# Performance work log

Measured on AMD Instinct MI355X. Metric: run time of the kernel, lower is better.

## Reference

```python
import jax, jax.numpy as jnp
import numpy as np

TEMPERATURE = 64.0


def setup_inputs() -> dict:
    key = jax.random.key(0)
    k1, k2 = jax.random.split(key)
    B, OUT, C = 256, 1000, 512
    x = jax.random.normal(k1, (B, 1, C), dtype=jnp.float32)
    # weight init: normal(0, sqrt(2/num_classes))
    weight = jax.random.normal(k2, (OUT, C), dtype=jnp.float32) * np.sqrt(2.0 / C).astype(np.float32)
    return {"x": x, "weight": weight, "num_batch": B}


def reference(x, weight, num_batch):
    # weight: (OUT, C) broadcast against x: (B, 1, C)
    # diff intermediate: (B, OUT, C); scores: (B, OUT)
    diff = weight[None, :, :] - x
    scores = -jnp.sum(diff * diff, axis=2) / TEMPERATURE
    return scores
```

## Files before the change

### kernel.cpp

```cpp
#include <hip/hip_runtime.h>
#include <hip/hip_bf16.h>


constexpr int OUTN = 1000;
constexpr int C_   = 512;

typedef __attribute__((ext_vector_type(8))) short bf16x8;
typedef __attribute__((ext_vector_type(4))) float f32x4;

__device__ __forceinline__ unsigned short f2bf(float f) {
    __hip_bfloat16 b = __float2bfloat16(f);
    return *reinterpret_cast<unsigned short*>(&b);
}

__global__ __launch_bounds__(512, 2)
void euc_mfma(const float* __restrict__ x, const float* __restrict__ w,
              float* __restrict__ out) {
    __shared__ unsigned short xs[32][512];
    __shared__ unsigned short ws[32][512];

    const int t    = threadIdx.x;
    const int lane = t & 63;
    const int wv   = t >> 6;
    const int rb   = blockIdx.y * 32;
    const int cb   = blockIdx.x * 32;

    #pragma unroll
    for (int i = 0; i < 8; ++i) {
        const int  row = 8 * (i & 3) + wv;
        const bool isx = (i < 4);
        float4 v0 = make_float4(0.f, 0.f, 0.f, 0.f), v1 = v0;
        if (isx) {
            const float* s = &x[(rb + row) * C_ + lane * 8];
            v0 = *(const float4*)s;  v1 = *(const float4*)(s + 4);
        } else if (cb + row < OUTN) {
            const float* s = &w[(cb + row) * C_ + lane * 8];
            v0 = *(const float4*)s;  v1 = *(const float4*)(s + 4);
        }
        union { unsigned short s[8]; int4 q; } u;
        u.s[0] = f2bf(v0.x); u.s[1] = f2bf(v0.y); u.s[2] = f2bf(v0.z); u.s[3] = f2bf(v0.w);
        u.s[4] = f2bf(v1.x); u.s[5] = f2bf(v1.y); u.s[6] = f2bf(v1.z); u.s[7] = f2bf(v1.w);
        const int g = lane ^ (row & 7);
        if (isx) *(int4*)&xs[row][g * 8] = u.q;
        else     *(int4*)&ws[row][g * 8] = u.q;
    }
    __syncthreads();

    const int q  = wv & 3, h = wv >> 2;
    const int qr = q >> 1, qc = q & 1;
    const int ra = 16 * qr + (lane & 15);
    const int rw = 16 * qc + (lane & 15);

    bf16x8 af[8], bf[8];
    f32x4 acc = {0.f, 0.f, 0.f, 0.f};
    #pragma unroll
    for (int i = 0; i < 8; ++i) {
        const int gi = 32 * h + 4 * i + (lane >> 4);
        af[i] = *(const bf16x8*)&xs[ra][(gi ^ (ra & 7)) * 8];
        bf[i] = *(const bf16x8*)&ws[rw][(gi ^ (rw & 7)) * 8];
        acc = __builtin_amdgcn_mfma_f32_16x16x32_bf16(af[i], bf[i], acc, 0, 0, 0);
    }

    const bool useA = (q == 0) || (q == 3);
    f32x4 nacc = {0.f, 0.f, 0.f, 0.f};
    if (useA) {
        #pragma unroll
        for (int i = 0; i < 8; ++i)
            nacc = __builtin_amdgcn_mfma_f32_16x16x32_bf16(af[i], af[i], nacc, 0, 0, 0);
    } else {
        #pragma unroll
        for (int i = 0; i < 8; ++i)
            nacc = __builtin_amdgcn_mfma_f32_16x16x32_bf16(bf[i], bf[i], nacc, 0, 0, 0);
    }

    __syncthreads();

    char* sbase = (char*)&xs[0][0];
    float* nb = (float*)(sbase + 4096);
    if (h == 1) *(f32x4*)(sbase + q * 1024 + lane * 16) = acc;
    {
        const int base = useA ? 16 * qr : 32 + 16 * qc;
        #pragma unroll
        for (int j = 0; j < 4; ++j) {
            const int r = (lane >> 4) * 4 + j;
            if ((lane & 15) == r) nb[h * 64 + base + r] = nacc[j];
        }
    }
    __syncthreads();

    if (h == 0) {
        const f32x4 p = *(const f32x4*)(sbase + q * 1024 + lane * 16);
        const int cl = 16 * qc + (lane & 15);
        const int c  = cb + cl;
        if (c < OUTN) {
            const float nw = nb[32 + cl] + nb[64 + 32 + cl];
            #pragma unroll
            for (int j = 0; j < 4; ++j) {
                const int r = 16 * qr + (lane >> 4) * 4 + j;
                const float nx = nb[r] + nb[64 + r];
                out[(rb + r) * OUTN + c] =
                    (2.f * (acc[j] + p[j]) - nx - nw) * 0.015625f;
            }
        }
    }
}

extern "C" void kernel_launch(void* const* d_in, const int* in_sizes, int n_in,
                              void* d_out, int out_size, void* d_ws, size_t ws_size,
                              hipStream_t stream) {
    const float* x = (const float*)d_in[0];
    const float* w = (const float*)d_in[1];
    float* out = (float*)d_out;

    dim3 grid((OUTN + 31) / 32, 256 / 32);
    dim3 block(512);
    euc_mfma<<<grid, block, 0, stream>>>(x, w, out);
}
```

Measured before the change: 9.816 us.

## Split K reduction across four wave groups with 1024-thread blocks

Doubles the block to 1024 threads so the 512-wide K dimension is split four ways (16 waves) instead of two, each wave doing half as many MFMAs and LDS reads. The staging loop is rewritten to a flat 4-iteration load over 1024 threads. Partial dot products and norms from the three extra K-slices are reduced through shared memory before the output write. This shortens per-wave serial work at the cost of more cross-wave reduction traffic and higher register and occupancy pressure per block.

```diff
diff --git a/kernel.cpp b/kernel.cpp
--- a/kernel.cpp
+++ b/kernel.cpp
@@ -13,7 +13,7 @@
     return *reinterpret_cast<unsigned short*>(&b);
 }
 
-__global__ __launch_bounds__(512, 2)
+__global__ __launch_bounds__(1024, 4)
 void euc_mfma(const float* __restrict__ x, const float* __restrict__ w,
               float* __restrict__ out) {
     __shared__ unsigned short xs[32][512];
@@ -26,23 +26,24 @@
     const int cb   = blockIdx.x * 32;
 
     #pragma unroll
-    for (int i = 0; i < 8; ++i) {
-        const int  row = 8 * (i & 3) + wv;
-        const bool isx = (i < 4);
+    for (int j = 0; j < 4; ++j) {
+        const int gidx = j * 1024 + t;
+        const int row  = gidx >> 6;
+        const int g    = gidx & 63;
         float4 v0 = make_float4(0.f, 0.f, 0.f, 0.f), v1 = v0;
-        if (isx) {
-            const float* s = &x[(rb + row) * C_ + lane * 8];
+        if (row < 32) {
+            const float* s = &x[(rb + row) * C_ + g * 8];
             v0 = *(const float4*)s;  v1 = *(const float4*)(s + 4);
-        } else if (cb + row < OUTN) {
-            const float* s = &w[(cb + row) * C_ + lane * 8];
+        } else if (cb + row - 32 < OUTN) {
+            const float* s = &w[(cb + row - 32) * C_ + g * 8];
             v0 = *(const float4*)s;  v1 = *(const float4*)(s + 4);
         }
         union { unsigned short s[8]; int4 q; } u;
         u.s[0] = f2bf(v0.x); u.s[1] = f2bf(v0.y); u.s[2] = f2bf(v0.z); u.s[3] = f2bf(v0.w);
         u.s[4] = f2bf(v1.x); u.s[5] = f2bf(v1.y); u.s[6] = f2bf(v1.z); u.s[7] = f2bf(v1.w);
-        const int g = lane ^ (row & 7);
-        if (isx) *(int4*)&xs[row][g * 8] = u.q;
-        else     *(int4*)&ws[row][g * 8] = u.q;
+        const int gs = (g ^ (row & 7)) * 8;
+        if (row < 32) *(int4*)&xs[row][gs]      = u.q;
+        else          *(int4*)&ws[row - 32][gs] = u.q;
     }
     __syncthreads();
 
@@ -51,33 +52,28 @@
     const int ra = 16 * qr + (lane & 15);
     const int rw = 16 * qc + (lane & 15);
 
-    bf16x8 af[8], bf[8];
+    bf16x8 af[4], bff[4];
     f32x4 acc = {0.f, 0.f, 0.f, 0.f};
     #pragma unroll
-    for (int i = 0; i < 8; ++i) {
-        const int gi = 32 * h + 4 * i + (lane >> 4);
-        af[i] = *(const bf16x8*)&xs[ra][(gi ^ (ra & 7)) * 8];
-        bf[i] = *(const bf16x8*)&ws[rw][(gi ^ (rw & 7)) * 8];
-        acc = __builtin_amdgcn_mfma_f32_16x16x32_bf16(af[i], bf[i], acc, 0, 0, 0);
+    for (int i = 0; i < 4; ++i) {
+        const int gi = 16 * h + 4 * i + (lane >> 4);
+        af[i]  = *(const bf16x8*)&xs[ra][(gi ^ (ra & 7)) * 8];
+        bff[i] = *(const bf16x8*)&ws[rw][(gi ^ (rw & 7)) * 8];
+        acc = __builtin_amdgcn_mfma_f32_16x16x32_bf16(af[i], bff[i], acc, 0, 0, 0);
     }
 
     const bool useA = (q == 0) || (q == 3);
     f32x4 nacc = {0.f, 0.f, 0.f, 0.f};
-    if (useA) {
-        #pragma unroll
-        for (int i = 0; i < 8; ++i)
-            nacc = __builtin_amdgcn_mfma_f32_16x16x32_bf16(af[i], af[i], nacc, 0, 0, 0);
-    } else {
-        #pragma unroll
-        for (int i = 0; i < 8; ++i)
-            nacc = __builtin_amdgcn_mfma_f32_16x16x32_bf16(bf[i], bf[i], nacc, 0, 0, 0);
+    #pragma unroll
+    for (int i = 0; i < 4; ++i) {
+        const bf16x8 f = useA ? af[i] : bff[i];
+        nacc = __builtin_amdgcn_mfma_f32_16x16x32_bf16(f, f, nacc, 0, 0, 0);
     }
-
     __syncthreads();
 
     char* sbase = (char*)&xs[0][0];
-    float* nb = (float*)(sbase + 4096);
-    if (h == 1) *(f32x4*)(sbase + q * 1024 + lane * 16) = acc;
+    if (h) *(f32x4*)(sbase + ((h - 1) * 4 + q) * 1024 + lane * 16) = acc;
+    float* nb = (float*)(sbase + 12288);
     {
         const int base = useA ? 16 * qr : 32 + 16 * qc;
         #pragma unroll
@@ -89,17 +85,20 @@
     __syncthreads();
 
     if (h == 0) {
-        const f32x4 p = *(const f32x4*)(sbase + q * 1024 + lane * 16);
+        #pragma unroll
+        for (int p = 0; p < 3; ++p) {
+            const f32x4 v = *(const f32x4*)(sbase + (p * 4 + q) * 1024 + lane * 16);
+            acc[0] += v[0]; acc[1] += v[1]; acc[2] += v[2]; acc[3] += v[3];
+        }
         const int cl = 16 * qc + (lane & 15);
         const int c  = cb + cl;
         if (c < OUTN) {
-            const float nw = nb[32 + cl] + nb[64 + 32 + cl];
+            const float nw = nb[32 + cl] + nb[64 + 32 + cl] + nb[128 + 32 + cl] + nb[192 + 32 + cl];
             #pragma unroll
             for (int j = 0; j < 4; ++j) {
                 const int r = 16 * qr + (lane >> 4) * 4 + j;
-                const float nx = nb[r] + nb[64 + r];
-                out[(rb + r) * OUTN + c] =
-                    (2.f * (acc[j] + p[j]) - nx - nw) * 0.015625f;
+                const float nx = nb[r] + nb[64 + r] + nb[128 + r] + nb[192 + r];
+                out[(rb + r) * OUTN + c] = (2.f * acc[j] - nx - nw) * 0.015625f;
             }
         }
     }
@@ -113,6 +112,6 @@
     float* out = (float*)d_out;
 
     dim3 grid((OUTN + 31) / 32, 256 / 32);
-    dim3 block(512);
+    dim3 block(1024);
     euc_mfma<<<grid, block, 0, stream>>>(x, w, out);
 }
```

Measured after the change: 9.785 us. About the same (-0.3%).
